# Optimization experiments

Hardware: AMD Instinct MI355X
Metric: run time of the kernel (lower is better)

## Reference

```python
import jax, jax.numpy as jnp
import numpy as np

HEADDIM = 128
CHUNK = 256


def _ssd_scan(x, dt, A, B, C, chunk):
    # x: (b,l,h,p)  dt: (b,l,h)  A: (h,)  B,C: (b,l,n)  (single group g=1 shared by all heads)
    b, l, h, p = x.shape
    n = B.shape[-1]
    nc = l // chunk
    dA = dt * A  # (b,l,h)
    xc = x.reshape(b, nc, chunk, h, p)
    dtc = dt.reshape(b, nc, chunk, h)
    dAc = dA.reshape(b, nc, chunk, h)
    Bc = B.reshape(b, nc, chunk, n)
    Cc = C.reshape(b, nc, chunk, n)
    cs = jnp.cumsum(dAc, axis=2)  # (b,nc,c,h) cumulative log-decay within chunk
    # intra-chunk quadratic part
    CB = jnp.einsum('bjin,bjkn->bjik', Cc, Bc)  # (b,nc,c,c)
    decay = jnp.exp(cs[:, :, :, None, :] - cs[:, :, None, :, :])  # (b,nc,i,k,h)
    mask = jnp.tril(jnp.ones((chunk, chunk), dtype=bool))
    decay = jnp.where(mask[None, None, :, :, None], decay, 0.0)
    y_intra = jnp.einsum('bjik,bjikh,bjkh,bjkhp->bjihp', CB, decay, dtc, xc)
    # per-chunk end states
    decay_states = jnp.exp(cs[:, :, -1:, :] - cs)  # (b,nc,c,h)
    states = jnp.einsum('bjkh,bjkh,bjkn,bjkhp->bjhnp', decay_states, dtc, Bc, xc)
    # recurrence across chunks: h_j = exp(sum dA_j) * h_{j-1} + states_j
    chunk_decay = jnp.exp(cs[:, :, -1, :])  # (b,nc,h)
    def step(carry, inp):
        s, d = inp
        new = carry * d[:, :, None, None] + s
        return new, carry  # emit state BEFORE this chunk
    init = jnp.zeros((b, h, n, p), x.dtype)
    _, prev = jax.lax.scan(step, init,
                           (states.transpose(1, 0, 2, 3, 4), chunk_decay.transpose(1, 0, 2)))
    prev = prev.transpose(1, 0, 2, 3, 4)  # (b,nc,h,n,p)
    y_inter = jnp.einsum('bjih,bjin,bjhnp->bjihp', jnp.exp(cs), Cc, prev)
    return (y_intra + y_inter).reshape(b, l, h, p)


def setup_inputs() -> dict:
    key = jax.random.key(0)
    k1, k2, k3, k4 = jax.random.split(key, 4)
    b, l, d_inner, nheads, d_state = 2, 4096, 2048, 16, 256
    x = jax.random.normal(k1, (b, l, d_inner), dtype=jnp.float32)
    BC = jax.random.normal(k2, (b, l, 2 * d_state), dtype=jnp.float32) * 0.1
    dt = jax.random.normal(k3, (b, l, 2 * nheads), dtype=jnp.float32) - 3.0
    A_log = jnp.zeros((nheads,), dtype=jnp.float32)
    D = jnp.ones((nheads,), dtype=jnp.float32)
    W_fcD = jax.random.normal(k4, (nheads, d_inner), dtype=jnp.float32) * 0.02
    return {"x": x, "BC": BC, "dt": dt, "A_log": A_log, "D": D, "W_fcD": W_fcD}


def reference(x, BC, dt, A_log, D, W_fcD):
    b, l, dim = x.shape
    h = A_log.shape[0]
    p = HEADDIM
    d_state = BC.shape[-1] // 2
    A = -jnp.exp(A_log)
    # bidirectional: concat forward stream with time-flipped backward stream along batch
    dt2 = jnp.concatenate((dt[:, :, :h], jnp.flip(dt[:, :, h:], axis=1)), axis=0)
    dt2 = jax.nn.softplus(dt2)
    x_og = x
    x2 = jnp.concatenate((x, jnp.flip(x, axis=1)), axis=0)
    BC2 = jnp.concatenate((BC, jnp.flip(BC, axis=1)), axis=0)
    B, C = BC2[..., :d_state], BC2[..., d_state:]
    y = _ssd_scan(x2.reshape(2 * b, l, h, p), dt2, A, B, C, CHUNK)
    y = y.reshape(2 * b, l, dim)
    y = jnp.roll(y, shift=1, axis=1).at[:, 0, :].set(0.0)
    y_fw, y_bw = y[:b], jnp.flip(y[b:], axis=1)
    gate = x_og @ W_fcD.T + D  # (b,l,h)
    y = y_fw + y_bw + x_og * jnp.repeat(gate, p, axis=-1)
    return y
```

## Files before the change

kernel.cpp:

```cpp
#include <hip/hip_runtime.h>
#include <stdint.h>

#define NB 2
#define SL 4096
#define NH 16
#define HD 128
#define DS 256
#define CK 256
#define NCH 16
#define NSQ 4
#define DI 2048

#define EPST 132

typedef unsigned short u16;
typedef unsigned int u32;
typedef __attribute__((ext_vector_type(8))) __bf16 bf16x8;
typedef __attribute__((ext_vector_type(4))) float f32x4;

__device__ __forceinline__ int tor(int dir, int t) { return dir ? (SL - 1 - t) : t; }

__device__ __forceinline__ u16 f2bf(float f) {
  u32 u = __float_as_uint(f);
  u = u + 0x7fffu + ((u >> 16) & 1u);
  return (u16)(u >> 16);
}
__device__ __forceinline__ float bf2f(u16 s) {
  return __uint_as_float(((u32)s) << 16);
}

__device__ __forceinline__ void gl_lds16(const u16* g, u16* l) {
  __builtin_amdgcn_global_load_lds((const __attribute__((address_space(1))) u32*)g,
                                   (__attribute__((address_space(3))) u32*)l, 16, 0, 0);
}

__device__ __forceinline__ void stage_tile(const u16* __restrict__ src, u16* lds,
                                           int lane, int w, int k0) {
  int sgrow = lane >> 2, sc = lane & 3;
  int r0 = w << 5;
  int ra = r0 + sgrow, rb = ra + 16;
  int kqa = (sc ^ ((ra >> 1) & 3)) << 3;
  int kqb = (sc ^ ((rb >> 1) & 3)) << 3;
  gl_lds16(src + (size_t)ra * 256 + k0 + kqa, lds + r0 * 32);
  gl_lds16(src + (size_t)rb * 256 + k0 + kqb, lds + (r0 + 16) * 32);
}

__device__ __forceinline__ bf16x8 frag(const u16* lds, int base_row, int m, int quad) {
  int row = base_row + m;
  return *(const bf16x8*)&lds[row * 32 + ((quad ^ ((row >> 1) & 3)) << 3)];
}

__device__ __forceinline__ void mfma16(const u16* As, const u16* Bs, int wi, int wp,
                                       int m, int quad, f32x4 acc[4][4]) {
  bf16x8 af[4], bv[4];
#pragma unroll
  for (int r = 0; r < 4; ++r) af[r] = frag(As, wi + (r << 4), m, quad);
#pragma unroll
  for (int c = 0; c < 4; ++c) bv[c] = frag(Bs, wp + (c << 4), m, quad);
#pragma unroll
  for (int r = 0; r < 4; ++r)
#pragma unroll
    for (int c = 0; c < 4; ++c)
      acc[r][c] = __builtin_amdgcn_mfma_f32_16x16x32_bf16(af[r], bv[c], acc[r][c], 0, 0, 0);
}

__global__ __launch_bounds__(256) void kprep(const float* __restrict__ dt,
                                             const float* __restrict__ A_log,
                                             float* __restrict__ csb,
                                             float* __restrict__ dtvb,
                                             float* __restrict__ cdecb) {
  int blk = blockIdx.x;
  int h = blk & 15, sj = blk >> 4;
  int s = sj >> 4, j = sj & 15;
  int b = s & 1, dir = s >> 1;
  int i = threadIdx.x;
  int to = tor(dir, j * CK + i);
  __shared__ float sbuf[CK];
  float a = -expf(A_log[h]);
  float raw = dt[((size_t)(b * SL + to)) * (2 * NH) + dir * NH + h];
  float sp = (raw > 20.f) ? raw : log1pf(expf(raw));
  sbuf[i] = sp * a;
  __syncthreads();
  for (int off = 1; off < CK; off <<= 1) {
    float v = (i >= off) ? sbuf[i - off] : 0.f;
    __syncthreads();
    sbuf[i] += v;
    __syncthreads();
  }
  float csv = sbuf[i];
  size_t base = ((size_t)sj * NH + h) * CK;
  csb[base + i] = csv;
  dtvb[base + i] = sp;
  if (i == CK - 1) cdecb[sj * NH + h] = expf(csv);
}

__global__ __launch_bounds__(256) void kcast(const float* __restrict__ BC,
                                             u16* __restrict__ Bbf,
                                             u16* __restrict__ Cbf) {
  int blk = blockIdx.x;
  int s = blk >> 12, t = blk & (SL - 1);
  int b = s & 1, dir = s >> 1;
  int tsrc = tor(dir, t);
  int tid = threadIdx.x;
  const float* src = BC + ((size_t)(b * SL + tsrc)) * (2 * DS);
  size_t dstb = ((size_t)s * SL + t) * DS;
  Bbf[dstb + tid] = f2bf(src[tid]);
  Cbf[dstb + tid] = f2bf(src[DS + tid]);
}

__global__ __launch_bounds__(256) void ktransB(const u16* __restrict__ Bbf,
                                               u16* __restrict__ BbfT) {
  int sj = blockIdx.x;
  int s = sj >> 4, j = sj & 15;
  __shared__ u16 T[64 * 264];
  int tid = threadIdx.x;
  const u16* src = Bbf + ((size_t)s * SL + j * CK) * DS;
  u16* dst = BbfT + (size_t)sj * DS * CK;
  int kr = tid >> 2, part = (tid & 3) * 64;
  for (int k0 = 0; k0 < CK; k0 += 64) {
    __syncthreads();
    {
      const uint4* gs = (const uint4*)(src + (size_t)(k0 + kr) * DS + part);
      uint4* tb = (uint4*)&T[kr * 264 + part];
#pragma unroll
      for (int q = 0; q < 8; ++q) tb[q] = gs[q];
    }
    __syncthreads();
    int n = tid;
    u16 col[64];
#pragma unroll
    for (int kq = 0; kq < 64; ++kq) col[kq] = T[kq * 264 + n];
    uint4* ds_ = (uint4*)(dst + (size_t)n * CK + k0);
#pragma unroll
    for (int q = 0; q < 8; ++q) {
      uint4 wv;
      wv.x = (u32)col[q * 8 + 0] | ((u32)col[q * 8 + 1] << 16);
      wv.y = (u32)col[q * 8 + 2] | ((u32)col[q * 8 + 3] << 16);
      wv.z = (u32)col[q * 8 + 4] | ((u32)col[q * 8 + 5] << 16);
      wv.w = (u32)col[q * 8 + 6] | ((u32)col[q * 8 + 7] << 16);
      ds_[q] = wv;
    }
  }
}

__global__ __launch_bounds__(256) void kxsT(const float* __restrict__ xg,
                                            const float* __restrict__ csb,
                                            const float* __restrict__ dtvb,
                                            u16* __restrict__ xsT) {
  int inst = blockIdx.x;
  int h = inst & 15, sj = inst >> 4;
  int s = sj >> 4, j = sj & 15;
  int b = s & 1, dir = s >> 1;
  int tid = threadIdx.x;
  __shared__ u16 Ls[128 * 40];
  size_t cbase = ((size_t)sj * NH + h) * CK;
  u16* dst = xsT + (size_t)inst * (128 * 256);
  int kk = tid >> 3;
  int pg = (tid & 7) * 16;
  int p2 = tid >> 1, half = tid & 1;
  for (int k0 = 0; k0 < CK; k0 += 32) {
    int kglob = k0 + kk;
    float sc_ = expf(-csb[cbase + kglob]) * dtvb[cbase + kglob];
    int t = tor(dir, j * CK + kglob);
    const float* src = xg + ((size_t)(b * SL + t)) * DI + h * HD + pg;
    float4 v0 = ((const float4*)src)[0];
    float4 v1 = ((const float4*)src)[1];
    float4 v2 = ((const float4*)src)[2];
    float4 v3 = ((const float4*)src)[3];
    float vv[16] = {v0.x, v0.y, v0.z, v0.w, v1.x, v1.y, v1.z, v1.w,
                    v2.x, v2.y, v2.z, v2.w, v3.x, v3.y, v3.z, v3.w};
    __syncthreads();
#pragma unroll
    for (int q = 0; q < 16; ++q) Ls[(pg + q) * 40 + kk] = f2bf(vv[q] * sc_);
    __syncthreads();
    uint4 w0 = *(const uint4*)&Ls[p2 * 40 + half * 16];
    uint4 w1 = *(const uint4*)&Ls[p2 * 40 + half * 16 + 8];
    *(uint4*)&dst[(size_t)p2 * 256 + k0 + half * 16] = w0;
    *(uint4*)&dst[(size_t)p2 * 256 + k0 + half * 16 + 8] = w1;
  }
}

__global__ __launch_bounds__(256) void kcb(const u16* __restrict__ Cbf,
                                           const u16* __restrict__ Bbf,
                                           u16* __restrict__ CBm) {
  int blk = blockIdx.x;
  int tri = blk % 3;
  int sj = blk / 3;
  int it0 = tri ? 128 : 0;
  int kt0 = (tri == 2) ? 128 : 0;
  int s = sj >> 4, j = sj & 15;
  __shared__ u16 smem[128 * EPST];
  u16* As = smem;
  u16* Bs = smem + 4096;
  int tid = threadIdx.x;
  int w = tid >> 6, lane = tid & 63;
  int wi = (w >> 1) << 6, wp = (w & 1) << 6;
  int m = lane & 15, quad = lane >> 4;
  const u16* Ab = Cbf + ((size_t)s * SL + j * CK + it0) * DS;
  const u16* Bb = Bbf + ((size_t)s * SL + j * CK + kt0) * DS;
  f32x4 zini = {0.f, 0.f, 0.f, 0.f};
  f32x4 acc[4][4];
#pragma unroll
  for (int r = 0; r < 4; ++r)
#pragma unroll
    for (int c = 0; c < 4; ++c) acc[r][c] = zini;
  for (int ks = 0; ks < 8; ++ks) {
    int k0 = ks << 5;
    stage_tile(Ab, As, lane, w, k0);
    stage_tile(Bb, Bs, lane, w, k0);
    __syncthreads();
    mfma16(As, Bs, wi, wp, m, quad, acc);
    __syncthreads();
  }
  int diag = (it0 == kt0);
#pragma unroll
  for (int r = 0; r < 4; ++r)
#pragma unroll
    for (int rg = 0; rg < 4; ++rg) {
      int irow = wi + (r << 4) + (quad << 2) + rg;
#pragma unroll
      for (int c = 0; c < 4; ++c) {
        int kcol = wp + (c << 4) + m;
        float v = acc[r][c][rg];
        if (diag && kcol > irow) v = 0.f;
        smem[irow * EPST + kcol] = f2bf(v);
      }
    }
  __syncthreads();
  {
    u16* dstb = CBm + ((size_t)sj * CK + it0) * CK + kt0;
    int rr = tid >> 1, off = (tid & 1) << 6;
    const uint4* srcv = (const uint4*)&smem[rr * EPST + off];
    uint4* dstv = (uint4*)(dstb + (size_t)rr * CK + off);
#pragma unroll
    for (int q = 0; q < 8; ++q) dstv[q] = srcv[q];
  }
}

__global__ __launch_bounds__(256) void kstates(const u16* __restrict__ xsT,
                                               const u16* __restrict__ BbfT,
                                               const float* __restrict__ cdecb,
                                               u16* __restrict__ prevT) {
  int blk = blockIdx.x;
  int ntile = blk & 1;
  int inst = blk >> 1;
  int h = inst & 15, sj = inst >> 4;
  int nt0 = ntile << 7;
  __shared__ u16 smem[128 * EPST];
  u16* As = smem;
  u16* Bs = smem + 4096;
  int tid = threadIdx.x;
  int w = tid >> 6, lane = tid & 63;
  int wi = (w >> 1) << 6, wp = (w & 1) << 6;
  int m = lane & 15, quad = lane >> 4;
  const u16* Ab = xsT + (size_t)inst * (128 * 256);
  const u16* Bb = BbfT + ((size_t)sj * DS + nt0) * CK;
  f32x4 zini = {0.f, 0.f, 0.f, 0.f};
  f32x4 acc[4][4];
#pragma unroll
  for (int r = 0; r < 4; ++r)
#pragma unroll
    for (int c = 0; c < 4; ++c) acc[r][c] = zini;
  for (int ks = 0; ks < 8; ++ks) {
    int k0 = ks << 5;
    stage_tile(Ab, As, lane, w, k0);
    stage_tile(Bb, Bs, lane, w, k0);
    __syncthreads();
    mfma16(As, Bs, wi, wp, m, quad, acc);
    __syncthreads();
  }
  float scale = cdecb[sj * NH + h];
#pragma unroll
  for (int r = 0; r < 4; ++r)
#pragma unroll
    for (int rg = 0; rg < 4; ++rg) {
      int prow = wi + (r << 4) + (quad << 2) + rg;
#pragma unroll
      for (int c = 0; c < 4; ++c) {
        int ncol = wp + (c << 4) + m;
        smem[prow * EPST + ncol] = f2bf(acc[r][c][rg] * scale);
      }
    }
  __syncthreads();
  {
    u16* dstb = prevT + (size_t)inst * (128 * 256) + nt0;
    int rr = tid >> 1, off = (tid & 1) << 6;
    const uint4* srcv = (const uint4*)&smem[rr * EPST + off];
    uint4* dstv = (uint4*)(dstb + (size_t)rr * 256 + off);
#pragma unroll
    for (int q = 0; q < 8; ++q) dstv[q] = srcv[q];
  }
}

__global__ __launch_bounds__(256) void kscan(u16* __restrict__ prevT,
                                             const float* __restrict__ cdecb) {
  int g = blockIdx.x * 256 + threadIdx.x;
  int n0 = (g & 31) * 8;
  int p = (g >> 5) & 127;
  int h = (g >> 12) & 15;
  int s = g >> 16;
  size_t base = ((size_t)(s * 256 + h) * 128 + p) * 256 + n0;
  const size_t stride = (size_t)NH * 128 * 256;
  float carry[8] = {0.f, 0.f, 0.f, 0.f, 0.f, 0.f, 0.f, 0.f};
  for (int j = 0; j < NCH; ++j) {
    size_t idx = base + (size_t)j * stride;
    uint4 u = *(const uint4*)&prevT[idx];
    u32 uu[4] = {u.x, u.y, u.z, u.w};
    float sv[8];
#pragma unroll
    for (int q = 0; q < 4; ++q) {
      sv[2 * q] = __uint_as_float(uu[q] << 16);
      sv[2 * q + 1] = __uint_as_float(uu[q] & 0xffff0000u);
    }
    uint4 wv;
    wv.x = (u32)f2bf(carry[0]) | ((u32)f2bf(carry[1]) << 16);
    wv.y = (u32)f2bf(carry[2]) | ((u32)f2bf(carry[3]) << 16);
    wv.z = (u32)f2bf(carry[4]) | ((u32)f2bf(carry[5]) << 16);
    wv.w = (u32)f2bf(carry[6]) | ((u32)f2bf(carry[7]) << 16);
    *(uint4*)&prevT[idx] = wv;
    float d = cdecb[(s * NCH + j) * NH + h];
#pragma unroll
    for (int q = 0; q < 8; ++q) carry[q] = carry[q] * d + sv[q];
  }
}

__global__ __launch_bounds__(256) void ky(const u16* __restrict__ CBm,
                                          const u16* __restrict__ Cbf,
                                          const u16* __restrict__ xsT,
                                          const u16* __restrict__ prevT,
                                          const float* __restrict__ csb,
                                          u16* __restrict__ ytmpb) {
  int blk = blockIdx.x;
  int itile = blk & 1;
  int inst = blk >> 1;
  int h = inst & 15, sj = inst >> 4;
  int s = sj >> 4, j = sj & 15;
  int it0 = itile << 7;
  __shared__ u16 smem[128 * EPST];
  u16* As = smem;
  u16* Bs = smem + 4096;
  int tid = threadIdx.x;
  int w = tid >> 6, lane = tid & 63;
  int wi = (w >> 1) << 6, wp = (w & 1) << 6;
  int m = lane & 15, quad = lane >> 4;

  const u16* Ai = CBm + ((size_t)sj * CK + it0) * CK;
  const u16* Ae = Cbf + ((size_t)s * SL + j * CK + it0) * DS;
  const u16* Bi = xsT + (size_t)inst * (128 * 256);
  const u16* Be = prevT + (size_t)inst * (128 * 256);

  int nIntra = itile ? 8 : 4;
  int nTot = nIntra + 8;

  f32x4 zini = {0.f, 0.f, 0.f, 0.f};
  f32x4 acc[4][4];
#pragma unroll
  for (int r = 0; r < 4; ++r)
#pragma unroll
    for (int c = 0; c < 4; ++c) acc[r][c] = zini;

  for (int ks = 0; ks < nTot; ++ks) {
    int intra = ks < nIntra;
    int k0 = (intra ? ks : ks - nIntra) << 5;
    const u16* Ab = intra ? Ai : Ae;
    const u16* Bb = intra ? Bi : Be;
    stage_tile(Ab, As, lane, w, k0);
    stage_tile(Bb, Bs, lane, w, k0);
    __syncthreads();
    mfma16(As, Bs, wi, wp, m, quad, acc);
    __syncthreads();
  }
  const float* csrow = csb + ((size_t)sj * NH + h) * CK + it0;
#pragma unroll
  for (int r = 0; r < 4; ++r)
#pragma unroll
    for (int rg = 0; rg < 4; ++rg) {
      int irow = wi + (r << 4) + (quad << 2) + rg;
      float esc = expf(csrow[irow]);
#pragma unroll
      for (int c = 0; c < 4; ++c) {
        int pcol = wp + (c << 4) + m;
        smem[irow * EPST + pcol] = f2bf(acc[r][c][rg] * esc);
      }
    }
  __syncthreads();
  {
    u16* yb = ytmpb + ((size_t)s * SL + j * CK + it0) * DI + h * HD;
    int rr = tid >> 1, off = (tid & 1) << 6;
    const uint4* srcv = (const uint4*)&smem[rr * EPST + off];
    uint4* dstv = (uint4*)(yb + (size_t)rr * DI + off);
#pragma unroll
    for (int q = 0; q < 8; ++q) dstv[q] = srcv[q];
  }
}

__global__ __launch_bounds__(256) void kwt(const float* __restrict__ Wg,
                                           float* __restrict__ WT) {
  int g = blockIdx.x * 256 + threadIdx.x;
  int d = g >> 4, h = g & 15;
  WT[g] = Wg[(size_t)h * DI + d];
}

__global__ __launch_bounds__(256) void kgate(const float* __restrict__ xg,
                                             const float* __restrict__ WT,
                                             const float* __restrict__ Dg,
                                             float* __restrict__ gate) {
  int wave = (blockIdx.x * 256 + threadIdx.x) >> 6;
  int lane = threadIdx.x & 63;
  int gg = lane >> 4, h = lane & 15;
  int row0 = wave * 8;
  const float* xb = xg + (size_t)row0 * DI;
  float acc[8] = {0.f, 0.f, 0.f, 0.f, 0.f, 0.f, 0.f, 0.f};
  for (int q = 0; q < 128; ++q) {
    int d = gg * 4 + 16 * q;
    float w0 = WT[(d + 0) * 16 + h];
    float w1 = WT[(d + 1) * 16 + h];
    float w2 = WT[(d + 2) * 16 + h];
    float w3 = WT[(d + 3) * 16 + h];
#pragma unroll
    for (int r = 0; r < 8; ++r) {
      float4 xv = *(const float4*)&xb[(size_t)r * DI + d];
      acc[r] += xv.x * w0 + xv.y * w1 + xv.z * w2 + xv.w * w3;
    }
  }
#pragma unroll
  for (int r = 0; r < 8; ++r) {
    acc[r] += __shfl_down(acc[r], 32);
    acc[r] += __shfl_down(acc[r], 16);
  }
  if (lane < 16) {
    float dv = Dg[h];
#pragma unroll
    for (int r = 0; r < 8; ++r) gate[(size_t)(row0 + r) * NH + h] = acc[r] + dv;
  }
}

__device__ __forceinline__ void unpk8(uint4 u, float* o) {
  o[0] = __uint_as_float(u.x << 16); o[1] = __uint_as_float(u.x & 0xffff0000u);
  o[2] = __uint_as_float(u.y << 16); o[3] = __uint_as_float(u.y & 0xffff0000u);
  o[4] = __uint_as_float(u.z << 16); o[5] = __uint_as_float(u.z & 0xffff0000u);
  o[6] = __uint_as_float(u.w << 16); o[7] = __uint_as_float(u.w & 0xffff0000u);
}

__global__ __launch_bounds__(256) void kcombine(const float* __restrict__ xg,
                                                const float* __restrict__ gate,
                                                const u16* __restrict__ ytmpb,
                                                float* __restrict__ out) {
  int bid = blockIdx.x;
  int b = bid >> 12;
  int t = bid & (SL - 1);
  int tid = threadIdx.x;
  int d0 = tid * 8;
  float g = gate[(size_t)(b * SL + t) * NH + (tid >> 4)];
  float fy[8] = {0.f, 0.f, 0.f, 0.f, 0.f, 0.f, 0.f, 0.f};
  float by[8] = {0.f, 0.f, 0.f, 0.f, 0.f, 0.f, 0.f, 0.f};
  if (t > 0) {
    uint4 u = *(const uint4*)(ytmpb + ((size_t)(b * SL + (t - 1))) * DI + d0);
    unpk8(u, fy);
  }
  if (t < SL - 1) {
    uint4 u = *(const uint4*)(ytmpb + ((size_t)((2 + b) * SL + (SL - 2 - t))) * DI + d0);
    unpk8(u, by);
  }
  const float* xr = xg + ((size_t)(b * SL + t)) * DI + d0;
  float4 x0 = ((const float4*)xr)[0];
  float4 x1 = ((const float4*)xr)[1];
  float xa[8] = {x0.x, x0.y, x0.z, x0.w, x1.x, x1.y, x1.z, x1.w};
  float* op = out + ((size_t)(b * SL + t)) * DI + d0;
  float4 o0, o1;
  o0.x = fy[0] + by[0] + xa[0] * g; o0.y = fy[1] + by[1] + xa[1] * g;
  o0.z = fy[2] + by[2] + xa[2] * g; o0.w = fy[3] + by[3] + xa[3] * g;
  o1.x = fy[4] + by[4] + xa[4] * g; o1.y = fy[5] + by[5] + xa[5] * g;
  o1.z = fy[6] + by[6] + xa[6] * g; o1.w = fy[7] + by[7] + xa[7] * g;
  ((float4*)op)[0] = o0;
  ((float4*)op)[1] = o1;
}

extern "C" void kernel_launch(void* const* d_in, const int* in_sizes, int n_in,
                              void* d_out, int out_size, void* d_ws, size_t ws_size,
                              hipStream_t stream) {
  (void)in_sizes; (void)n_in; (void)out_size; (void)ws_size;
  const float* x     = (const float*)d_in[0];
  const float* BC    = (const float*)d_in[1];
  const float* dt    = (const float*)d_in[2];
  const float* A_log = (const float*)d_in[3];
  const float* Dg    = (const float*)d_in[4];
  const float* W     = (const float*)d_in[5];
  float* out = (float*)d_out;

  char* p = (char*)d_ws;
  float* cs   = (float*)p;  p += (size_t)NSQ * NCH * NH * CK * 4;
  float* dtv  = (float*)p;  p += (size_t)NSQ * NCH * NH * CK * 4;
  float* cdec = (float*)p;  p += (size_t)NSQ * NCH * NH * 4;
  float* WT   = (float*)p;  p += (size_t)DI * NH * 4;
  float* gateb= (float*)p;  p += (size_t)NB * SL * NH * 4;
  u16* Bbf    = (u16*)p;    p += (size_t)NSQ * SL * DS * 2;
  u16* Cbf    = (u16*)p;    p += (size_t)NSQ * SL * DS * 2;
  u16* BbfT   = (u16*)p;    p += (size_t)NSQ * NCH * DS * CK * 2;
  u16* CBm    = (u16*)p;    p += (size_t)NSQ * NCH * CK * CK * 2;
  u16* xsT    = (u16*)p;    p += (size_t)NSQ * NCH * NH * HD * CK * 2;
  u16* prevT  = (u16*)p;    p += (size_t)NSQ * NCH * NH * HD * DS * 2;
  u16* ytmpb  = (u16*)p;    p += (size_t)NSQ * SL * DI * 2;

  hipLaunchKernelGGL(kprep,   dim3(NSQ * NCH * NH),      dim3(CK),  0, stream, dt, A_log, cs, dtv, cdec);
  hipLaunchKernelGGL(kcast,   dim3(NSQ * SL),            dim3(256), 0, stream, BC, Bbf, Cbf);
  hipLaunchKernelGGL(ktransB, dim3(NSQ * NCH),           dim3(256), 0, stream, Bbf, BbfT);
  hipLaunchKernelGGL(kxsT,    dim3(NSQ * NCH * NH),      dim3(256), 0, stream, x, cs, dtv, xsT);
  hipLaunchKernelGGL(kcb,     dim3(NSQ * NCH * 3),       dim3(256), 0, stream, Cbf, Bbf, CBm);
  hipLaunchKernelGGL(kwt,     dim3(DI * NH / 256),       dim3(256), 0, stream, W, WT);
  hipLaunchKernelGGL(kgate,   dim3(NB * SL / 32),        dim3(256), 0, stream, x, WT, Dg, gateb);
  hipLaunchKernelGGL(kstates, dim3(NSQ * NCH * NH * 2),  dim3(256), 0, stream, xsT, BbfT, cdec, prevT);
  hipLaunchKernelGGL(kscan,   dim3(NSQ * NH * HD * DS / (256 * 8)), dim3(256), 0, stream, prevT, cdec);
  hipLaunchKernelGGL(ky,      dim3(NSQ * NCH * NH * 2),  dim3(256), 0, stream, CBm, Cbf, xsT, prevT, cs, ytmpb);
  hipLaunchKernelGGL(kcombine,dim3(NB * SL),             dim3(256), 0, stream, x, gateb, ytmpb, out);
}
```

Before: 420.1 us.

## Double-buffer GEMM tiles via register prefetch and prefetch loads in xsT and scan

Replaces the direct global-to-LDS async loads in the three MFMA GEMM kernels with register-staged loads into double-buffered LDS. The next tile's global load is issued while the current tile is computed, and each k-step needs one barrier instead of two. The xsT transpose kernel and the chunk scan kernel also prefetch the next iteration's global data into registers. The cost is higher register pressure and extra LDS store instructions in place of the async LDS load path.

```diff
diff --git a/kernel.cpp b/kernel.cpp
--- a/kernel.cpp
+++ b/kernel.cpp
@@ -29,20 +29,16 @@
   return __uint_as_float(((u32)s) << 16);
 }
 
-__device__ __forceinline__ void gl_lds16(const u16* g, u16* l) {
-  __builtin_amdgcn_global_load_lds((const __attribute__((address_space(1))) u32*)g,
-                                   (__attribute__((address_space(3))) u32*)l, 16, 0, 0);
-}
-
-__device__ __forceinline__ void stage_tile(const u16* __restrict__ src, u16* lds,
-                                           int lane, int w, int k0) {
-  int sgrow = lane >> 2, sc = lane & 3;
-  int r0 = w << 5;
-  int ra = r0 + sgrow, rb = ra + 16;
-  int kqa = (sc ^ ((ra >> 1) & 3)) << 3;
-  int kqb = (sc ^ ((rb >> 1) & 3)) << 3;
-  gl_lds16(src + (size_t)ra * 256 + k0 + kqa, lds + r0 * 32);
-  gl_lds16(src + (size_t)rb * 256 + k0 + kqb, lds + (r0 + 16) * 32);
+struct Stg { uint4 a, b; };
+
+__device__ __forceinline__ Stg ld_tile(const u16* __restrict__ src, int row, int q0, int k0) {
+  const uint4* p = (const uint4*)(src + (size_t)row * 256 + k0 + (q0 << 3));
+  Stg s; s.a = p[0]; s.b = p[1]; return s;
+}
+__device__ __forceinline__ void st_tile(u16* buf, int row, int q0, Stg s) {
+  int sw = (row >> 1) & 3;
+  *(uint4*)&buf[row * 32 + ((q0 ^ sw) << 3)] = s.a;
+  *(uint4*)&buf[row * 32 + (((q0 + 1) ^ sw) << 3)] = s.b;
 }
 
 __device__ __forceinline__ bf16x8 frag(const u16* lds, int base_row, int m, int quad) {
@@ -158,20 +154,27 @@
   int kk = tid >> 3;
   int pg = (tid & 7) * 16;
   int p2 = tid >> 1, half = tid & 1;
+  float4 v[4];
+  {
+    int t = tor(dir, j * CK + kk);
+    const float* src = xg + ((size_t)(b * SL + t)) * DI + h * HD + pg;
+    v[0] = ((const float4*)src)[0]; v[1] = ((const float4*)src)[1];
+    v[2] = ((const float4*)src)[2]; v[3] = ((const float4*)src)[3];
+  }
   for (int k0 = 0; k0 < CK; k0 += 32) {
     int kglob = k0 + kk;
     float sc_ = expf(-csb[cbase + kglob]) * dtvb[cbase + kglob];
-    int t = tor(dir, j * CK + kglob);
-    const float* src = xg + ((size_t)(b * SL + t)) * DI + h * HD + pg;
-    float4 v0 = ((const float4*)src)[0];
-    float4 v1 = ((const float4*)src)[1];
-    float4 v2 = ((const float4*)src)[2];
-    float4 v3 = ((const float4*)src)[3];
-    float vv[16] = {v0.x, v0.y, v0.z, v0.w, v1.x, v1.y, v1.z, v1.w,
-                    v2.x, v2.y, v2.z, v2.w, v3.x, v3.y, v3.z, v3.w};
+    float vv[16] = {v[0].x, v[0].y, v[0].z, v[0].w, v[1].x, v[1].y, v[1].z, v[1].w,
+                    v[2].x, v[2].y, v[2].z, v[2].w, v[3].x, v[3].y, v[3].z, v[3].w};
     __syncthreads();
 #pragma unroll
     for (int q = 0; q < 16; ++q) Ls[(pg + q) * 40 + kk] = f2bf(vv[q] * sc_);
+    if (k0 + 32 < CK) {
+      int t = tor(dir, j * CK + k0 + 32 + kk);
+      const float* src = xg + ((size_t)(b * SL + t)) * DI + h * HD + pg;
+      v[0] = ((const float4*)src)[0]; v[1] = ((const float4*)src)[1];
+      v[2] = ((const float4*)src)[2]; v[3] = ((const float4*)src)[3];
+    }
     __syncthreads();
     uint4 w0 = *(const uint4*)&Ls[p2 * 40 + half * 16];
     uint4 w1 = *(const uint4*)&Ls[p2 * 40 + half * 16 + 8];
@@ -190,12 +193,11 @@
   int kt0 = (tri == 2) ? 128 : 0;
   int s = sj >> 4, j = sj & 15;
   __shared__ u16 smem[128 * EPST];
-  u16* As = smem;
-  u16* Bs = smem + 4096;
   int tid = threadIdx.x;
   int w = tid >> 6, lane = tid & 63;
   int wi = (w >> 1) << 6, wp = (w & 1) << 6;
   int m = lane & 15, quad = lane >> 4;
+  int row = tid >> 1, q0 = (tid & 1) << 1;
   const u16* Ab = Cbf + ((size_t)s * SL + j * CK + it0) * DS;
   const u16* Bb = Bbf + ((size_t)s * SL + j * CK + kt0) * DS;
   f32x4 zini = {0.f, 0.f, 0.f, 0.f};
@@ -204,14 +206,31 @@
   for (int r = 0; r < 4; ++r)
 #pragma unroll
     for (int c = 0; c < 4; ++c) acc[r][c] = zini;
-  for (int ks = 0; ks < 8; ++ks) {
-    int k0 = ks << 5;
-    stage_tile(Ab, As, lane, w, k0);
-    stage_tile(Bb, Bs, lane, w, k0);
-    __syncthreads();
-    mfma16(As, Bs, wi, wp, m, quad, acc);
-    __syncthreads();
-  }
+  const int n = 8;
+  Stg pa = ld_tile(Ab, row, q0, 0);
+  Stg pb = ld_tile(Bb, row, q0, 0);
+  st_tile(smem, row, q0, pa);
+  st_tile(smem + 8192, row, q0, pb);
+  pa = ld_tile(Ab, row, q0, 32);
+  pb = ld_tile(Bb, row, q0, 32);
+  for (int ks = 1; ks < n; ++ks) {
+    __syncthreads();
+    int cur = (ks & 1) << 12;
+    st_tile(smem + cur, row, q0, pa);
+    st_tile(smem + 8192 + cur, row, q0, pb);
+    if (ks + 1 < n) {
+      pa = ld_tile(Ab, row, q0, (ks + 1) << 5);
+      pb = ld_tile(Bb, row, q0, (ks + 1) << 5);
+    }
+    int prv = ((ks - 1) & 1) << 12;
+    mfma16(smem + prv, smem + 8192 + prv, wi, wp, m, quad, acc);
+  }
+  __syncthreads();
+  {
+    int prv = ((n - 1) & 1) << 12;
+    mfma16(smem + prv, smem + 8192 + prv, wi, wp, m, quad, acc);
+  }
+  __syncthreads();
   int diag = (it0 == kt0);
 #pragma unroll
   for (int r = 0; r < 4; ++r)
@@ -247,12 +266,11 @@
   int h = inst & 15, sj = inst >> 4;
   int nt0 = ntile << 7;
   __shared__ u16 smem[128 * EPST];
-  u16* As = smem;
-  u16* Bs = smem + 4096;
   int tid = threadIdx.x;
   int w = tid >> 6, lane = tid & 63;
   int wi = (w >> 1) << 6, wp = (w & 1) << 6;
   int m = lane & 15, quad = lane >> 4;
+  int row = tid >> 1, q0 = (tid & 1) << 1;
   const u16* Ab = xsT + (size_t)inst * (128 * 256);
   const u16* Bb = BbfT + ((size_t)sj * DS + nt0) * CK;
   f32x4 zini = {0.f, 0.f, 0.f, 0.f};
@@ -261,14 +279,31 @@
   for (int r = 0; r < 4; ++r)
 #pragma unroll
     for (int c = 0; c < 4; ++c) acc[r][c] = zini;
-  for (int ks = 0; ks < 8; ++ks) {
-    int k0 = ks << 5;
-    stage_tile(Ab, As, lane, w, k0);
-    stage_tile(Bb, Bs, lane, w, k0);
-    __syncthreads();
-    mfma16(As, Bs, wi, wp, m, quad, acc);
-    __syncthreads();
-  }
+  const int n = 8;
+  Stg pa = ld_tile(Ab, row, q0, 0);
+  Stg pb = ld_tile(Bb, row, q0, 0);
+  st_tile(smem, row, q0, pa);
+  st_tile(smem + 8192, row, q0, pb);
+  pa = ld_tile(Ab, row, q0, 32);
+  pb = ld_tile(Bb, row, q0, 32);
+  for (int ks = 1; ks < n; ++ks) {
+    __syncthreads();
+    int cur = (ks & 1) << 12;
+    st_tile(smem + cur, row, q0, pa);
+    st_tile(smem + 8192 + cur, row, q0, pb);
+    if (ks + 1 < n) {
+      pa = ld_tile(Ab, row, q0, (ks + 1) << 5);
+      pb = ld_tile(Bb, row, q0, (ks + 1) << 5);
+    }
+    int prv = ((ks - 1) & 1) << 12;
+    mfma16(smem + prv, smem + 8192 + prv, wi, wp, m, quad, acc);
+  }
+  __syncthreads();
+  {
+    int prv = ((n - 1) & 1) << 12;
+    mfma16(smem + prv, smem + 8192 + prv, wi, wp, m, quad, acc);
+  }
+  __syncthreads();
   float scale = cdecb[sj * NH + h];
 #pragma unroll
   for (int r = 0; r < 4; ++r)
@@ -302,9 +337,11 @@
   size_t base = ((size_t)(s * 256 + h) * 128 + p) * 256 + n0;
   const size_t stride = (size_t)NH * 128 * 256;
   float carry[8] = {0.f, 0.f, 0.f, 0.f, 0.f, 0.f, 0.f, 0.f};
+  uint4 u = *(const uint4*)&prevT[base];
   for (int j = 0; j < NCH; ++j) {
     size_t idx = base + (size_t)j * stride;
-    uint4 u = *(const uint4*)&prevT[idx];
+    uint4 un;
+    if (j + 1 < NCH) un = *(const uint4*)&prevT[idx + stride];
     u32 uu[4] = {u.x, u.y, u.z, u.w};
     float sv[8];
 #pragma unroll
@@ -321,6 +358,7 @@
     float d = cdecb[(s * NCH + j) * NH + h];
 #pragma unroll
     for (int q = 0; q < 8; ++q) carry[q] = carry[q] * d + sv[q];
+    u = un;
   }
 }
 
@@ -337,12 +375,11 @@
   int s = sj >> 4, j = sj & 15;
   int it0 = itile << 7;
   __shared__ u16 smem[128 * EPST];
-  u16* As = smem;
-  u16* Bs = smem + 4096;
   int tid = threadIdx.x;
   int w = tid >> 6, lane = tid & 63;
   int wi = (w >> 1) << 6, wp = (w & 1) << 6;
   int m = lane & 15, quad = lane >> 4;
+  int row = tid >> 1, q0 = (tid & 1) << 1;
 
   const u16* Ai = CBm + ((size_t)sj * CK + it0) * CK;
   const u16* Ae = Cbf + ((size_t)s * SL + j * CK + it0) * DS;
@@ -350,7 +387,7 @@
   const u16* Be = prevT + (size_t)inst * (128 * 256);
 
   int nIntra = itile ? 8 : 4;
-  int nTot = nIntra + 8;
+  int n = nIntra + 8;
 
   f32x4 zini = {0.f, 0.f, 0.f, 0.f};
   f32x4 acc[4][4];
@@ -359,17 +396,44 @@
 #pragma unroll
     for (int c = 0; c < 4; ++c) acc[r][c] = zini;
 
-  for (int ks = 0; ks < nTot; ++ks) {
-    int intra = ks < nIntra;
-    int k0 = (intra ? ks : ks - nIntra) << 5;
-    const u16* Ab = intra ? Ai : Ae;
-    const u16* Bb = intra ? Bi : Be;
-    stage_tile(Ab, As, lane, w, k0);
-    stage_tile(Bb, Bs, lane, w, k0);
-    __syncthreads();
-    mfma16(As, Bs, wi, wp, m, quad, acc);
-    __syncthreads();
-  }
+#define KY_SRC(ks, Ap, Bp, kk)                                  \
+  {                                                             \
+    int intra_ = (ks) < nIntra;                                 \
+    kk = (intra_ ? (ks) : (ks) - nIntra) << 5;                  \
+    Ap = intra_ ? Ai : Ae;                                      \
+    Bp = intra_ ? Bi : Be;                                      \
+  }
+
+  const u16 *Ap, *Bp; int kk;
+  KY_SRC(0, Ap, Bp, kk);
+  Stg pa = ld_tile(Ap, row, q0, kk);
+  Stg pb = ld_tile(Bp, row, q0, kk);
+  st_tile(smem, row, q0, pa);
+  st_tile(smem + 8192, row, q0, pb);
+  KY_SRC(1, Ap, Bp, kk);
+  pa = ld_tile(Ap, row, q0, kk);
+  pb = ld_tile(Bp, row, q0, kk);
+  for (int ks = 1; ks < n; ++ks) {
+    __syncthreads();
+    int cur = (ks & 1) << 12;
+    st_tile(smem + cur, row, q0, pa);
+    st_tile(smem + 8192 + cur, row, q0, pb);
+    if (ks + 1 < n) {
+      KY_SRC(ks + 1, Ap, Bp, kk);
+      pa = ld_tile(Ap, row, q0, kk);
+      pb = ld_tile(Bp, row, q0, kk);
+    }
+    int prv = ((ks - 1) & 1) << 12;
+    mfma16(smem + prv, smem + 8192 + prv, wi, wp, m, quad, acc);
+  }
+  __syncthreads();
+  {
+    int prv = ((n - 1) & 1) << 12;
+    mfma16(smem + prv, smem + 8192 + prv, wi, wp, m, quad, acc);
+  }
+  __syncthreads();
+#undef KY_SRC
+
   const float* csrow = csb + ((size_t)sj * NH + h) * CK + it0;
 #pragma unroll
   for (int r = 0; r < 4; ++r)
```

After: 418.6 us. Within noise of the previous version (-0.3%).
